# Kernel optimization log

Measured on AMD Instinct MI355X. Metric: run time of the kernel, lower is better.

Reference implementation:

```python
import jax, jax.numpy as jnp
import numpy as np

B, S, H, F, E, TOPK = 2, 1024, 1024, 2816, 8, 2

def setup_inputs() -> dict:
    key = jax.random.key(0)
    k1, k2, k3, k4 = jax.random.split(key, 4)
    return {
        "hidden_states": jax.random.normal(k1, (B, S, H), dtype=jnp.float32),
        "gate_w": jax.random.normal(k2, (E, H), dtype=jnp.float32) * 0.02,  # gate 1x1 conv == [E,H] matrix
        "w1": jax.random.normal(k3, (E, F, H), dtype=jnp.float32) * 0.02,   # per-expert up-proj
        "w2": jax.random.normal(k4, (E, H, F), dtype=jnp.float32) * 0.02,   # per-expert down-proj
        "top_k": TOPK,
    }

def reference(hidden_states, gate_w, w1, w2, top_k):
    b, s, h = hidden_states.shape
    e = gate_w.shape[0]
    x = hidden_states.reshape(-1, h)                       # [N, H]
    n = x.shape[0]
    # Router: 1x1 conv gate == linear, softmax, top-k, renormalize
    logits = x @ gate_w.T                                  # [N, E]
    probs = jax.nn.softmax(logits, axis=-1)
    topw, topi = jax.lax.top_k(probs, top_k)               # [N, k]
    topw = topw / jnp.sum(topw, axis=-1, keepdims=True)
    # Per-(token, expert) combine weight; zero for non-selected experts.
    # Equivalent to torch.where(topk_indices == e, topk_weights, 0).sum(-1).
    comb = jnp.zeros((n, e), dtype=x.dtype).at[jnp.arange(n)[:, None], topi].add(topw)  # [N, E]
    # Expert MLPs (1x1 convs == GEMMs): up -> SiLU -> down, weighted combine.
    up = jnp.einsum('nh,efh->nef', x, w1)                  # [N, E, F]
    act = jax.nn.silu(up)
    out = jnp.einsum('nef,ehf->neh', act, w2)              # [N, E, H]
    y = jnp.einsum('ne,neh->nh', comb, out)                # weighted combine
    return y.reshape(b, s, h)
```

## Files before the change

kernel.cpp:

```cpp
#include <hip/hip_runtime.h>
#include <stdint.h>

#define N_TOK 2048
#define H_DIM 1024
#define F_DIM 2816
#define N_EXP 8
#define NSLOT (N_TOK * 2)

#define BK 64
#define KSPLIT 2
#define KHALF (F_DIM / KSPLIT)
#define MAX_TILES 40

#define NU_W (N_EXP * F_DIM * H_DIM / 8)

typedef __attribute__((ext_vector_type(8))) short bf16x8;
typedef __attribute__((ext_vector_type(4))) float f32x4;

typedef __attribute__((address_space(1))) unsigned int gu32;
typedef __attribute__((address_space(3))) unsigned int lu32;

static __device__ __forceinline__ unsigned short f2bf(float f) {
    union { float f; unsigned u; } v; v.f = f;
    unsigned r = v.u + 0x7fffu + ((v.u >> 16) & 1u);
    return (unsigned short)(r >> 16);
}

static __device__ __forceinline__ void gload16(const unsigned short* g, unsigned short* l) {
    __builtin_amdgcn_global_load_lds((const gu32*)g, (lu32*)l, 16, 0, 0);
}

static __device__ __forceinline__ void conv8(const float* __restrict__ src,
                                             unsigned short* __restrict__ dst, long k)
{
    const float4 a = *(const float4*)(src + k * 8);
    const float4 b = *(const float4*)(src + k * 8 + 4);
    uint4 o;
    o.x = (unsigned)f2bf(a.x) | ((unsigned)f2bf(a.y) << 16);
    o.y = (unsigned)f2bf(a.z) | ((unsigned)f2bf(a.w) << 16);
    o.z = (unsigned)f2bf(b.x) | ((unsigned)f2bf(b.y) << 16);
    o.w = (unsigned)f2bf(b.z) | ((unsigned)f2bf(b.w) << 16);
    *(uint4*)(dst + k * 8) = o;
}

__global__ __launch_bounds__(256) void convert_w_kernel(
    const float* __restrict__ w1, const float* __restrict__ w2,
    unsigned short* __restrict__ w1_bf, unsigned short* __restrict__ w2_bf)
{
    const long total = 2L * NU_W;
    long u = ((long)blockIdx.x * 256 + threadIdx.x) * 2;
    const long stride = (long)gridDim.x * 256 * 2;
    for (; u < total; u += stride) {
        const float* src = (u < NU_W) ? w1 : w2;
        unsigned short* dst = (u < NU_W) ? w1_bf : w2_bf;
        const long k = (u < NU_W) ? u : u - NU_W;
        conv8(src, dst, k);
        conv8(src, dst, k + 1);
    }
}

__global__ __launch_bounds__(256) void router_kernel(
    const float* __restrict__ x, const float* __restrict__ gate_w,
    int* __restrict__ counts, int* __restrict__ row_token, float* __restrict__ row_weight,
    int* __restrict__ slot_e, int* __restrict__ slot_pos,
    unsigned short* __restrict__ x_bf)
{
    __shared__ float gsm[N_EXP * H_DIM];
    for (int i = threadIdx.x; i < N_EXP * H_DIM / 4; i += 256)
        ((float4*)gsm)[i] = ((const float4*)gate_w)[i];
    __syncthreads();

    const int wave = threadIdx.x >> 6;
    const int lane = threadIdx.x & 63;
    const int n = blockIdx.x * 4 + wave;
    if (n >= N_TOK) return;

    const float4* xrow = (const float4*)(x + (size_t)n * H_DIM);
    float4 xv[4];
#pragma unroll
    for (int i = 0; i < 4; i++) xv[i] = xrow[lane + 64 * i];

#pragma unroll
    for (int i = 0; i < 4; i++) {
        ushort4 b;
        b.x = f2bf(xv[i].x); b.y = f2bf(xv[i].y); b.z = f2bf(xv[i].z); b.w = f2bf(xv[i].w);
        *(ushort4*)(x_bf + (size_t)n * H_DIM + (lane + 64 * i) * 4) = b;
    }

    float logit[N_EXP];
#pragma unroll
    for (int e = 0; e < N_EXP; e++) {
        float p = 0.f;
#pragma unroll
        for (int i = 0; i < 4; i++) {
            const float4 g = ((const float4*)gsm)[e * 256 + lane + 64 * i];
            p += xv[i].x * g.x + xv[i].y * g.y + xv[i].z * g.z + xv[i].w * g.w;
        }
#pragma unroll
        for (int s = 32; s > 0; s >>= 1) p += __shfl_xor(p, s, 64);
        logit[e] = p;
    }

    if (lane == 0) {
        int e0 = 0; float l0 = logit[0];
#pragma unroll
        for (int e = 1; e < N_EXP; e++) if (logit[e] > l0) { l0 = logit[e]; e0 = e; }
        int e1 = -1; float l1 = -3.4e38f;
#pragma unroll
        for (int e = 0; e < N_EXP; e++) if (e != e0 && logit[e] > l1) { l1 = logit[e]; e1 = e; }
        float w0 = 1.f / (1.f + __expf(l1 - l0));
        float w1 = 1.f - w0;
        int p0 = atomicAdd(&counts[e0], 1);
        int p1 = atomicAdd(&counts[e1], 1);
        row_token[e0 * N_TOK + p0] = n;  row_weight[e0 * N_TOK + p0] = w0;
        row_token[e1 * N_TOK + p1] = n;  row_weight[e1 * N_TOK + p1] = w1;
        slot_e[n * 2 + 0] = e0;  slot_pos[n * 2 + 0] = p0;
        slot_e[n * 2 + 1] = e1;  slot_pos[n * 2 + 1] = p1;
    }
}

__global__ void scan_kernel(const int* __restrict__ counts, int* __restrict__ offsets,
                            int* __restrict__ tile_e, int* __restrict__ tile_m,
                            int* __restrict__ ntiles)
{
    if (threadIdx.x == 0 && blockIdx.x == 0) {
        int acc = 0, t = 0;
        for (int e = 0; e < N_EXP; e++) {
            offsets[e] = acc; acc += counts[e];
            const int nt = (counts[e] + 127) >> 7;
            for (int m = 0; m < nt; m++) { tile_e[t] = e; tile_m[t] = m; t++; }
        }
        *ntiles = t;
    }
}

__global__ __launch_bounds__(256) void up_gemm_kernel(
    const unsigned short* __restrict__ x_bf, const unsigned short* __restrict__ w1_bf,
    const int* __restrict__ counts, const int* __restrict__ offsets,
    const int* __restrict__ tile_e, const int* __restrict__ tile_m,
    const int* __restrict__ ntiles,
    const int* __restrict__ row_token,
    unsigned short* __restrict__ act)
{
    const int slot = blockIdx.y;
    if (slot >= *ntiles) return;
    const int e = tile_e[slot];
    const int mTile = tile_m[slot];
    const int cnt = counts[e];
    const int fTile = blockIdx.x;
    const int off = offsets[e];

    __shared__ __align__(16) unsigned short As[128 * 64];
    __shared__ __align__(16) unsigned short Bs[128 * 64];

    const int tid = threadIdx.x;
    const int lane = tid & 63;
    const int wave = tid >> 6;
    const int wm = (wave >> 1) * 64, wn = (wave & 1) * 64;

    const unsigned short* aSrc[4];
    const unsigned short* bSrc[4];
#pragma unroll
    for (int j = 0; j < 4; j++) {
        const int row_local = wave * 32 + j * 8 + (lane >> 3);
        const int pos = mTile * 128 + row_local;
        const int tok = row_token[e * N_TOK + min(pos, cnt - 1)];
        aSrc[j] = x_bf + (size_t)tok * H_DIM + (lane & 7) * 8;
        bSrc[j] = w1_bf + ((size_t)e * F_DIM + fTile * 128 + row_local) * H_DIM + (lane & 7) * 8;
    }

    f32x4 acc[4][4];
#pragma unroll
    for (int i = 0; i < 4; i++)
#pragma unroll
        for (int j = 0; j < 4; j++) acc[i][j] = (f32x4)(0.f);

    const int NKT = H_DIM / BK;
    for (int kt = 0; kt < NKT; kt++) {
        const int koff = kt * BK;
#pragma unroll
        for (int j = 0; j < 4; j++) {
            gload16(aSrc[j] + koff, As + (wave * 4 + j) * 512);
            gload16(bSrc[j] + koff, Bs + (wave * 4 + j) * 512);
        }
        __syncthreads();
#pragma unroll
        for (int kk = 0; kk < BK / 32; kk++) {
            const int kloc = kk * 32 + (lane >> 4) * 8;
            bf16x8 af[4], bfr[4];
#pragma unroll
            for (int i = 0; i < 4; i++)
                af[i] = *(const bf16x8*)(As + (wm + i * 16 + (lane & 15)) * 64 + kloc);
#pragma unroll
            for (int i = 0; i < 4; i++)
                bfr[i] = *(const bf16x8*)(Bs + (wn + i * 16 + (lane & 15)) * 64 + kloc);
#pragma unroll
            for (int i = 0; i < 4; i++)
#pragma unroll
                for (int j = 0; j < 4; j++)
                    acc[i][j] = __builtin_amdgcn_mfma_f32_16x16x32_bf16(af[i], bfr[j], acc[i][j], 0, 0, 0);
        }
        __syncthreads();
    }

#pragma unroll
    for (int i = 0; i < 4; i++) {
        const int mrow = wm + i * 16 + ((lane >> 4) << 2);
#pragma unroll
        for (int r = 0; r < 4; r++) {
            const int m = mTile * 128 + mrow + r;
            if (m < cnt) {
#pragma unroll
                for (int j = 0; j < 4; j++) {
                    float v = acc[i][j][r];
                    float s = v / (1.f + __expf(-v));
                    int col = fTile * 128 + wn + j * 16 + (lane & 15);
                    act[(size_t)(off + m) * F_DIM + col] = f2bf(s);
                }
            }
        }
    }
}

__global__ __launch_bounds__(256) void down_gemm_kernel(
    const unsigned short* __restrict__ act, const unsigned short* __restrict__ w2_bf,
    const int* __restrict__ counts, const int* __restrict__ offsets,
    const int* __restrict__ tile_e, const int* __restrict__ tile_m,
    const int* __restrict__ ntiles,
    const float* __restrict__ row_weight,
    float* __restrict__ out_partial)
{
    const int slot = blockIdx.y;
    if (slot >= *ntiles) return;
    const int e = tile_e[slot];
    const int mTile = tile_m[slot];
    const int ks = blockIdx.z;
    const int cnt = counts[e];
    const int hTile = blockIdx.x;
    const int off = offsets[e];
    const int kbase = ks * KHALF;

    __shared__ __align__(16) unsigned short As[128 * 64];
    __shared__ __align__(16) unsigned short Bs[128 * 64];

    const int tid = threadIdx.x;
    const int lane = tid & 63;
    const int wave = tid >> 6;
    const int wm = (wave >> 1) * 64, wn = (wave & 1) * 64;

    const unsigned short* aSrc[4];
    const unsigned short* bSrc[4];
#pragma unroll
    for (int j = 0; j < 4; j++) {
        const int row_local = wave * 32 + j * 8 + (lane >> 3);
        const int slotRow = off + min(mTile * 128 + row_local, cnt - 1);
        aSrc[j] = act + (size_t)slotRow * F_DIM + kbase + (lane & 7) * 8;
        bSrc[j] = w2_bf + ((size_t)e * H_DIM + hTile * 128 + row_local) * F_DIM + kbase + (lane & 7) * 8;
    }

    f32x4 acc[4][4];
#pragma unroll
    for (int i = 0; i < 4; i++)
#pragma unroll
        for (int j = 0; j < 4; j++) acc[i][j] = (f32x4)(0.f);

    const int NKT = KHALF / BK;
    for (int kt = 0; kt < NKT; kt++) {
        const int koff = kt * BK;
#pragma unroll
        for (int j = 0; j < 4; j++) {
            gload16(aSrc[j] + koff, As + (wave * 4 + j) * 512);
            gload16(bSrc[j] + koff, Bs + (wave * 4 + j) * 512);
        }
        __syncthreads();
#pragma unroll
        for (int kk = 0; kk < BK / 32; kk++) {
            const int kloc = kk * 32 + (lane >> 4) * 8;
            bf16x8 af[4], bfr[4];
#pragma unroll
            for (int i = 0; i < 4; i++)
                af[i] = *(const bf16x8*)(As + (wm + i * 16 + (lane & 15)) * 64 + kloc);
#pragma unroll
            for (int i = 0; i < 4; i++)
                bfr[i] = *(const bf16x8*)(Bs + (wn + i * 16 + (lane & 15)) * 64 + kloc);
#pragma unroll
            for (int i = 0; i < 4; i++)
#pragma unroll
                for (int j = 0; j < 4; j++)
                    acc[i][j] = __builtin_amdgcn_mfma_f32_16x16x32_bf16(af[i], bfr[j], acc[i][j], 0, 0, 0);
        }
        __syncthreads();
    }

    float* obase = out_partial + (size_t)ks * NSLOT * H_DIM;
#pragma unroll
    for (int i = 0; i < 4; i++) {
        const int mrow = wm + i * 16 + ((lane >> 4) << 2);
#pragma unroll
        for (int r = 0; r < 4; r++) {
            const int m = mTile * 128 + mrow + r;
            if (m < cnt) {
                const float w = row_weight[e * N_TOK + m];
#pragma unroll
                for (int j = 0; j < 4; j++) {
                    int col = hTile * 128 + wn + j * 16 + (lane & 15);
                    obase[(size_t)(off + m) * H_DIM + col] = w * acc[i][j][r];
                }
            }
        }
    }
}

__global__ __launch_bounds__(256) void combine_kernel(
    const float* __restrict__ out_partial, const int* __restrict__ offsets,
    const int* __restrict__ slot_e, const int* __restrict__ slot_pos,
    float* __restrict__ out)
{
    const int n = blockIdx.x;
    const int r0 = offsets[slot_e[n * 2 + 0]] + slot_pos[n * 2 + 0];
    const int r1 = offsets[slot_e[n * 2 + 1]] + slot_pos[n * 2 + 1];
    const int t = threadIdx.x;
    const float* p0 = out_partial;
    const float* p1 = out_partial + (size_t)NSLOT * H_DIM;
    const float4 a = *(const float4*)(p0 + (size_t)r0 * H_DIM + t * 4);
    const float4 b = *(const float4*)(p1 + (size_t)r0 * H_DIM + t * 4);
    const float4 c = *(const float4*)(p0 + (size_t)r1 * H_DIM + t * 4);
    const float4 d = *(const float4*)(p1 + (size_t)r1 * H_DIM + t * 4);
    float4 s;
    s.x = (a.x + b.x) + (c.x + d.x);
    s.y = (a.y + b.y) + (c.y + d.y);
    s.z = (a.z + b.z) + (c.z + d.z);
    s.w = (a.w + b.w) + (c.w + d.w);
    *(float4*)(out + (size_t)n * H_DIM + t * 4) = s;
}

extern "C" void kernel_launch(void* const* d_in, const int* in_sizes, int n_in,
                              void* d_out, int out_size, void* d_ws, size_t ws_size,
                              hipStream_t stream) {
    const float* x      = (const float*)d_in[0];
    const float* gate_w = (const float*)d_in[1];
    const float* w1     = (const float*)d_in[2];
    const float* w2     = (const float*)d_in[3];
    float* out = (float*)d_out;

    char* ws = (char*)d_ws;
    size_t o = 0;
    auto alloc = [&](size_t bytes) -> void* {
        void* p = ws + o;
        o = (o + bytes + 255) & ~(size_t)255;
        return p;
    };
    int*   counts     = (int*)  alloc(N_EXP * sizeof(int));
    int*   offsets    = (int*)  alloc(N_EXP * sizeof(int));
    int*   tile_e     = (int*)  alloc(MAX_TILES * sizeof(int));
    int*   tile_m     = (int*)  alloc(MAX_TILES * sizeof(int));
    int*   ntiles     = (int*)  alloc(sizeof(int));
    int*   row_token  = (int*)  alloc((size_t)N_EXP * N_TOK * sizeof(int));
    float* row_weight = (float*)alloc((size_t)N_EXP * N_TOK * sizeof(float));
    int*   slot_e     = (int*)  alloc((size_t)N_TOK * 2 * sizeof(int));
    int*   slot_pos   = (int*)  alloc((size_t)N_TOK * 2 * sizeof(int));
    unsigned short* act = (unsigned short*)alloc((size_t)NSLOT * F_DIM * sizeof(unsigned short));
    float* out_partial = (float*)alloc((size_t)KSPLIT * NSLOT * H_DIM * sizeof(float));
    unsigned short* x_bf  = (unsigned short*)alloc((size_t)N_TOK * H_DIM * sizeof(unsigned short));
    unsigned short* w1_bf = (unsigned short*)alloc((size_t)N_EXP * F_DIM * H_DIM * sizeof(unsigned short));
    unsigned short* w2_bf = (unsigned short*)alloc((size_t)N_EXP * H_DIM * F_DIM * sizeof(unsigned short));

    hipMemsetAsync(counts, 0, N_EXP * sizeof(int), stream);

    router_kernel<<<N_TOK / 4, 256, 0, stream>>>(x, gate_w, counts, row_token, row_weight, slot_e, slot_pos, x_bf);
    scan_kernel<<<1, 64, 0, stream>>>(counts, offsets, tile_e, tile_m, ntiles);
    convert_w_kernel<<<4096, 256, 0, stream>>>(w1, w2, w1_bf, w2_bf);
    up_gemm_kernel<<<dim3(F_DIM / 128, MAX_TILES), 256, 0, stream>>>(
        x_bf, w1_bf, counts, offsets, tile_e, tile_m, ntiles, row_token, act);
    down_gemm_kernel<<<dim3(H_DIM / 128, MAX_TILES, KSPLIT), 256, 0, stream>>>(
        act, w2_bf, counts, offsets, tile_e, tile_m, ntiles, row_weight, out_partial);
    combine_kernel<<<N_TOK, 256, 0, stream>>>(out_partial, offsets, slot_e, slot_pos, out);
}
```

Measured before the change: 397.9 us.

## Enlarge expert GEMM M-tile to 256 rows with 512-thread blocks

Both expert GEMMs now use 256x128 tiles computed by 8 waves (each 128x32), so each block reuses the loaded weight tile across twice as many token rows. This halves redundant weight streaming from global memory and reduces the tile count, with MAX_TILES dropping to 24. The weight conversion kernel now processes one float4 per thread iteration on a smaller grid. The risks are more padding waste on partial expert tiles, fewer blocks in flight, and higher per-wave A-fragment LDS reads.

```diff
diff --git a/kernel.cpp b/kernel.cpp
--- a/kernel.cpp
+++ b/kernel.cpp
@@ -10,9 +10,7 @@
 #define BK 64
 #define KSPLIT 2
 #define KHALF (F_DIM / KSPLIT)
-#define MAX_TILES 40
-
-#define NU_W (N_EXP * F_DIM * H_DIM / 8)
+#define MAX_TILES 24
 
 typedef __attribute__((ext_vector_type(8))) short bf16x8;
 typedef __attribute__((ext_vector_type(4))) float f32x4;
@@ -30,32 +28,21 @@
     __builtin_amdgcn_global_load_lds((const gu32*)g, (lu32*)l, 16, 0, 0);
 }
 
-static __device__ __forceinline__ void conv8(const float* __restrict__ src,
-                                             unsigned short* __restrict__ dst, long k)
-{
-    const float4 a = *(const float4*)(src + k * 8);
-    const float4 b = *(const float4*)(src + k * 8 + 4);
-    uint4 o;
-    o.x = (unsigned)f2bf(a.x) | ((unsigned)f2bf(a.y) << 16);
-    o.y = (unsigned)f2bf(a.z) | ((unsigned)f2bf(a.w) << 16);
-    o.z = (unsigned)f2bf(b.x) | ((unsigned)f2bf(b.y) << 16);
-    o.w = (unsigned)f2bf(b.z) | ((unsigned)f2bf(b.w) << 16);
-    *(uint4*)(dst + k * 8) = o;
-}
-
 __global__ __launch_bounds__(256) void convert_w_kernel(
     const float* __restrict__ w1, const float* __restrict__ w2,
     unsigned short* __restrict__ w1_bf, unsigned short* __restrict__ w2_bf)
 {
-    const long total = 2L * NU_W;
-    long u = ((long)blockIdx.x * 256 + threadIdx.x) * 2;
-    const long stride = (long)gridDim.x * 256 * 2;
-    for (; u < total; u += stride) {
-        const float* src = (u < NU_W) ? w1 : w2;
-        unsigned short* dst = (u < NU_W) ? w1_bf : w2_bf;
-        const long k = (u < NU_W) ? u : u - NU_W;
-        conv8(src, dst, k);
-        conv8(src, dst, k + 1);
+    const long NU4 = (long)N_EXP * F_DIM * H_DIM / 4;
+    const long total = 2 * NU4;
+    for (long u = (long)blockIdx.x * 256 + threadIdx.x; u < total; u += (long)gridDim.x * 256) {
+        const float* src = (u < NU4) ? w1 : w2;
+        unsigned short* dst = (u < NU4) ? w1_bf : w2_bf;
+        const long k = (u < NU4) ? u : u - NU4;
+        const float4 v = *(const float4*)(src + k * 4);
+        uint2 o;
+        o.x = (unsigned)f2bf(v.x) | ((unsigned)f2bf(v.y) << 16);
+        o.y = (unsigned)f2bf(v.z) | ((unsigned)f2bf(v.w) << 16);
+        *(uint2*)(dst + k * 4) = o;
     }
 }
 
@@ -127,14 +114,14 @@
         int acc = 0, t = 0;
         for (int e = 0; e < N_EXP; e++) {
             offsets[e] = acc; acc += counts[e];
-            const int nt = (counts[e] + 127) >> 7;
+            const int nt = (counts[e] + 255) >> 8;
             for (int m = 0; m < nt; m++) { tile_e[t] = e; tile_m[t] = m; t++; }
         }
         *ntiles = t;
     }
 }
 
-__global__ __launch_bounds__(256) void up_gemm_kernel(
+__global__ __launch_bounds__(512, 2) void up_gemm_kernel(
     const unsigned short* __restrict__ x_bf, const unsigned short* __restrict__ w1_bf,
     const int* __restrict__ counts, const int* __restrict__ offsets,
     const int* __restrict__ tile_e, const int* __restrict__ tile_m,
@@ -150,68 +137,74 @@
     const int fTile = blockIdx.x;
     const int off = offsets[e];
 
-    __shared__ __align__(16) unsigned short As[128 * 64];
+    __shared__ __align__(16) unsigned short As[256 * 64];
     __shared__ __align__(16) unsigned short Bs[128 * 64];
 
     const int tid = threadIdx.x;
     const int lane = tid & 63;
     const int wave = tid >> 6;
-    const int wm = (wave >> 1) * 64, wn = (wave & 1) * 64;
+    const int wm = (wave >> 2) * 128;
+    const int wn = (wave & 3) * 32;
 
     const unsigned short* aSrc[4];
-    const unsigned short* bSrc[4];
+    const unsigned short* bSrc[2];
 #pragma unroll
     for (int j = 0; j < 4; j++) {
         const int row_local = wave * 32 + j * 8 + (lane >> 3);
-        const int pos = mTile * 128 + row_local;
+        const int pos = mTile * 256 + row_local;
         const int tok = row_token[e * N_TOK + min(pos, cnt - 1)];
         aSrc[j] = x_bf + (size_t)tok * H_DIM + (lane & 7) * 8;
+    }
+#pragma unroll
+    for (int j = 0; j < 2; j++) {
+        const int row_local = wave * 16 + j * 8 + (lane >> 3);
         bSrc[j] = w1_bf + ((size_t)e * F_DIM + fTile * 128 + row_local) * H_DIM + (lane & 7) * 8;
     }
 
-    f32x4 acc[4][4];
-#pragma unroll
-    for (int i = 0; i < 4; i++)
-#pragma unroll
-        for (int j = 0; j < 4; j++) acc[i][j] = (f32x4)(0.f);
+    f32x4 acc[8][2];
+#pragma unroll
+    for (int i = 0; i < 8; i++)
+#pragma unroll
+        for (int j = 0; j < 2; j++) acc[i][j] = (f32x4)(0.f);
 
     const int NKT = H_DIM / BK;
     for (int kt = 0; kt < NKT; kt++) {
         const int koff = kt * BK;
 #pragma unroll
-        for (int j = 0; j < 4; j++) {
+        for (int j = 0; j < 4; j++)
             gload16(aSrc[j] + koff, As + (wave * 4 + j) * 512);
-            gload16(bSrc[j] + koff, Bs + (wave * 4 + j) * 512);
-        }
+#pragma unroll
+        for (int j = 0; j < 2; j++)
+            gload16(bSrc[j] + koff, Bs + (wave * 2 + j) * 512);
         __syncthreads();
 #pragma unroll
         for (int kk = 0; kk < BK / 32; kk++) {
             const int kloc = kk * 32 + (lane >> 4) * 8;
-            bf16x8 af[4], bfr[4];
-#pragma unroll
-            for (int i = 0; i < 4; i++)
+            bf16x8 af[8], bfr[2];
+#pragma unroll
+            for (int i = 0; i < 8; i++)
                 af[i] = *(const bf16x8*)(As + (wm + i * 16 + (lane & 15)) * 64 + kloc);
 #pragma unroll
-            for (int i = 0; i < 4; i++)
-                bfr[i] = *(const bf16x8*)(Bs + (wn + i * 16 + (lane & 15)) * 64 + kloc);
-#pragma unroll
-            for (int i = 0; i < 4; i++)
-#pragma unroll
-                for (int j = 0; j < 4; j++)
+            for (int j = 0; j < 2; j++)
+                bfr[j] = *(const bf16x8*)(Bs + (wn + j * 16 + (lane & 15)) * 64 + kloc);
+#pragma unroll
+            for (int i = 0; i < 8; i++)
+#pragma unroll
+                for (int j = 0; j < 2; j++)
                     acc[i][j] = __builtin_amdgcn_mfma_f32_16x16x32_bf16(af[i], bfr[j], acc[i][j], 0, 0, 0);
         }
         __syncthreads();
     }
 
 #pragma unroll
-    for (int i = 0; i < 4; i++) {
+    for (int i = 0; i < 8; i++) {
         const int mrow = wm + i * 16 + ((lane >> 4) << 2);
 #pragma unroll
         for (int r = 0; r < 4; r++) {
-            const int m = mTile * 128 + mrow + r;
+            const int m = mTile * 256 + mrow + r;
             if (m < cnt) {
 #pragma unroll
-                for (int j = 0; j < 4; j++) {
+                for (int j = 0; j < 2; j++) {
                     float v = acc[i][j][r];
                     float s = v / (1.f + __expf(-v));
                     int col = fTile * 128 + wn + j * 16 + (lane & 15);
@@ -222,7 +215,7 @@
     }
 }
 
-__global__ __launch_bounds__(256) void down_gemm_kernel(
+__global__ __launch_bounds__(512, 2) void down_gemm_kernel(
     const unsigned short* __restrict__ act, const unsigned short* __restrict__ w2_bf,
     const int* __restrict__ counts, const int* __restrict__ offsets,
     const int* __restrict__ tile_e, const int* __restrict__ tile_m,
@@ -240,53 +233,59 @@
     const int off = offsets[e];
     const int kbase = ks * KHALF;
 
-    __shared__ __align__(16) unsigned short As[128 * 64];
+    __shared__ __align__(16) unsigned short As[256 * 64];
     __shared__ __align__(16) unsigned short Bs[128 * 64];
 
     const int tid = threadIdx.x;
     const int lane = tid & 63;
     const int wave = tid >> 6;
-    const int wm = (wave >> 1) * 64, wn = (wave & 1) * 64;
+    const int wm = (wave >> 2) * 128;
+    const int wn = (wave & 3) * 32;
 
     const unsigned short* aSrc[4];
-    const unsigned short* bSrc[4];
+    const unsigned short* bSrc[2];
 #pragma unroll
     for (int j = 0; j < 4; j++) {
         const int row_local = wave * 32 + j * 8 + (lane >> 3);
-        const int slotRow = off + min(mTile * 128 + row_local, cnt - 1);
+        const int slotRow = off + min(mTile * 256 + row_local, cnt - 1);
         aSrc[j] = act + (size_t)slotRow * F_DIM + kbase + (lane & 7) * 8;
+    }
+#pragma unroll
+    for (int j = 0; j < 2; j++) {
+        const int row_local = wave * 16 + j * 8 + (lane >> 3);
         bSrc[j] = w2_bf + ((size_t)e * H_DIM + hTile * 128 + row_local) * F_DIM + kbase + (lane & 7) * 8;
     }
 
-    f32x4 acc[4][4];
-#pragma unroll
-    for (int i = 0; i < 4; i++)
-#pragma unroll
-        for (int j = 0; j < 4; j++) acc[i][j] = (f32x4)(0.f);
+    f32x4 acc[8][2];
+#pragma unroll
+    for (int i = 0; i < 8; i++)
+#pragma unroll
+        for (int j = 0; j < 2; j++) acc[i][j] = (f32x4)(0.f);
 
     const int NKT = KHALF / BK;
     for (int kt = 0; kt < NKT; kt++) {
         const int koff = kt * BK;
 #pragma unroll
-        for (int j = 0; j < 4; j++) {
+        for (int j = 0; j < 4; j++)
             gload16(aSrc[j] + koff, As + (wave * 4 + j) * 512);
-            gload16(bSrc[j] + koff, Bs + (wave * 4 + j) * 512);
-        }
+#pragma unroll
+        for (int j = 0; j < 2; j++)
+            gload16(bSrc[j] + koff, Bs + (wave * 2 + j) * 512);
         __syncthreads();
 #pragma unroll
         for (int kk = 0; kk < BK / 32; kk++) {
             const int kloc = kk * 32 + (lane >> 4) * 8;
-            bf16x8 af[4], bfr[4];
-#pragma unroll
-            for (int i = 0; i < 4; i++)
+            bf16x8 af[8], bfr[2];
+#pragma unroll
+            for (int i = 0; i < 8; i++)
                 af[i] = *(const bf16x8*)(As + (wm + i * 16 + (lane & 15)) * 64 + kloc);
 #pragma unroll
-            for (int i = 0; i < 4; i++)
-                bfr[i] = *(const bf16x8*)(Bs + (wn + i * 16 + (lane & 15)) * 64 + kloc);
-#pragma unroll
-            for (int i = 0; i < 4; i++)
-#pragma unroll
-                for (int j = 0; j < 4; j++)
+            for (int j = 0; j < 2; j++)
+                bfr[j] = *(const bf16x8*)(Bs + (wn + j * 16 + (lane & 15)) * 64 + kloc);
+#pragma unroll
+            for (int i = 0; i < 8; i++)
+#pragma unroll
+                for (int j = 0; j < 2; j++)
                     acc[i][j] = __builtin_amdgcn_mfma_f32_16x16x32_bf16(af[i], bfr[j], acc[i][j], 0, 0, 0);
         }
         __syncthreads();
@@ -294,15 +293,15 @@
 
     float* obase = out_partial + (size_t)ks * NSLOT * H_DIM;
 #pragma unroll
-    for (int i = 0; i < 4; i++) {
+    for (int i = 0; i < 8; i++) {
         const int mrow = wm + i * 16 + ((lane >> 4) << 2);
 #pragma unroll
         for (int r = 0; r < 4; r++) {
-            const int m = mTile * 128 + mrow + r;
+            const int m = mTile * 256 + mrow + r;
             if (m < cnt) {
                 const float w = row_weight[e * N_TOK + m];
 #pragma unroll
-                for (int j = 0; j < 4; j++) {
+                for (int j = 0; j < 2; j++) {
                     int col = hTile * 128 + wn + j * 16 + (lane & 15);
                     obase[(size_t)(off + m) * H_DIM + col] = w * acc[i][j][r];
                 }
@@ -369,10 +368,10 @@
 
     router_kernel<<<N_TOK / 4, 256, 0, stream>>>(x, gate_w, counts, row_token, row_weight, slot_e, slot_pos, x_bf);
     scan_kernel<<<1, 64, 0, stream>>>(counts, offsets, tile_e, tile_m, ntiles);
-    convert_w_kernel<<<4096, 256, 0, stream>>>(w1, w2, w1_bf, w2_bf);
-    up_gemm_kernel<<<dim3(F_DIM / 128, MAX_TILES), 256, 0, stream>>>(
+    convert_w_kernel<<<2048, 256, 0, stream>>>(w1, w2, w1_bf, w2_bf);
+    up_gemm_kernel<<<dim3(F_DIM / 128, MAX_TILES), 512, 0, stream>>>(
         x_bf, w1_bf, counts, offsets, tile_e, tile_m, ntiles, row_token, act);
-    down_gemm_kernel<<<dim3(H_DIM / 128, MAX_TILES, KSPLIT), 256, 0, stream>>>(
+    down_gemm_kernel<<<dim3(H_DIM / 128, MAX_TILES, KSPLIT), 512, 0, stream>>>(
         act, w2_bf, counts, offsets, tile_e, tile_m, ntiles, row_weight, out_partial);
     combine_kernel<<<N_TOK, 256, 0, stream>>>(out_partial, offsets, slot_e, slot_pos, out);
 }
```

Measured after the change: 414.3 us. 1.04x slower.

## Double-buffer LDS in expert GEMMs and fold scan into weight conversion

Applied to the files above, without the earlier changes.

Both up and down expert GEMMs now prefetch the next K tile into a second LDS buffer while computing on the current one, with raised wave priority around the MFMA section. The separate single-thread scan kernel is merged into the weight-conversion kernel, removing one launch, and the conversion loop is reworked to process float4 chunks with a halved grid. This aims to hide global-to-LDS latency behind matrix math, at the cost of doubling LDS per block, which may lower occupancy.

```diff
diff --git a/kernel.cpp b/kernel.cpp
--- a/kernel.cpp
+++ b/kernel.cpp
@@ -12,8 +12,6 @@
 #define KHALF (F_DIM / KSPLIT)
 #define MAX_TILES 40
 
-#define NU_W (N_EXP * F_DIM * H_DIM / 8)
-
 typedef __attribute__((ext_vector_type(8))) short bf16x8;
 typedef __attribute__((ext_vector_type(4))) float f32x4;
 
@@ -30,32 +28,53 @@
     __builtin_amdgcn_global_load_lds((const gu32*)g, (lu32*)l, 16, 0, 0);
 }
 
-static __device__ __forceinline__ void conv8(const float* __restrict__ src,
-                                             unsigned short* __restrict__ dst, long k)
-{
-    const float4 a = *(const float4*)(src + k * 8);
-    const float4 b = *(const float4*)(src + k * 8 + 4);
-    uint4 o;
-    o.x = (unsigned)f2bf(a.x) | ((unsigned)f2bf(a.y) << 16);
-    o.y = (unsigned)f2bf(a.z) | ((unsigned)f2bf(a.w) << 16);
-    o.z = (unsigned)f2bf(b.x) | ((unsigned)f2bf(b.y) << 16);
-    o.w = (unsigned)f2bf(b.z) | ((unsigned)f2bf(b.w) << 16);
-    *(uint4*)(dst + k * 8) = o;
-}
-
 __global__ __launch_bounds__(256) void convert_w_kernel(
     const float* __restrict__ w1, const float* __restrict__ w2,
-    unsigned short* __restrict__ w1_bf, unsigned short* __restrict__ w2_bf)
+    unsigned short* __restrict__ w1_bf, unsigned short* __restrict__ w2_bf,
+    const int* __restrict__ counts, int* __restrict__ offsets,
+    int* __restrict__ tile_e, int* __restrict__ tile_m, int* __restrict__ ntiles)
 {
-    const long total = 2L * NU_W;
-    long u = ((long)blockIdx.x * 256 + threadIdx.x) * 2;
-    const long stride = (long)gridDim.x * 256 * 2;
-    for (; u < total; u += stride) {
-        const float* src = (u < NU_W) ? w1 : w2;
-        unsigned short* dst = (u < NU_W) ? w1_bf : w2_bf;
-        const long k = (u < NU_W) ? u : u - NU_W;
-        conv8(src, dst, k);
-        conv8(src, dst, k + 1);
+    if (blockIdx.x == 0 && threadIdx.x == 0) {
+        int acc = 0, t = 0;
+        for (int e = 0; e < N_EXP; e++) {
+            offsets[e] = acc; acc += counts[e];
+            const int nt = (counts[e] + 127) >> 7;
+            for (int m = 0; m < nt; m++) { tile_e[t] = e; tile_m[t] = m; t++; }
+        }
+        *ntiles = t;
+    }
+
+    const long NU4 = (long)N_EXP * F_DIM * H_DIM / 4;
+    const long total = 2 * NU4;
+    long u = (long)blockIdx.x * 256 + threadIdx.x;
+    const long stride = (long)gridDim.x * 256;
+    for (; u + stride < total; u += 2 * stride) {
+        const long u1 = u + stride;
+        const float* s0 = (u  < NU4) ? w1 : w2;
+        const float* s1 = (u1 < NU4) ? w1 : w2;
+        unsigned short* d0 = (u  < NU4) ? w1_bf : w2_bf;
+        unsigned short* d1 = (u1 < NU4) ? w1_bf : w2_bf;
+        const long k0 = (u  < NU4) ? u  : u  - NU4;
+        const long k1 = (u1 < NU4) ? u1 : u1 - NU4;
+        const float4 v0 = *(const float4*)(s0 + k0 * 4);
+        const float4 v1 = *(const float4*)(s1 + k1 * 4);
+        uint2 o0, o1;
+        o0.x = (unsigned)f2bf(v0.x) | ((unsigned)f2bf(v0.y) << 16);
+        o0.y = (unsigned)f2bf(v0.z) | ((unsigned)f2bf(v0.w) << 16);
+        o1.x = (unsigned)f2bf(v1.x) | ((unsigned)f2bf(v1.y) << 16);
+        o1.y = (unsigned)f2bf(v1.z) | ((unsigned)f2bf(v1.w) << 16);
+        *(uint2*)(d0 + k0 * 4) = o0;
+        *(uint2*)(d1 + k1 * 4) = o1;
+    }
+    if (u < total) {
+        const float* s = (u < NU4) ? w1 : w2;
+        unsigned short* d = (u < NU4) ? w1_bf : w2_bf;
+        const long k = (u < NU4) ? u : u - NU4;
+        const float4 v = *(const float4*)(s + k * 4);
+        uint2 o;
+        o.x = (unsigned)f2bf(v.x) | ((unsigned)f2bf(v.y) << 16);
+        o.y = (unsigned)f2bf(v.z) | ((unsigned)f2bf(v.w) << 16);
+        *(uint2*)(d + k * 4) = o;
     }
 }
 
@@ -116,21 +135,6 @@
         row_token[e1 * N_TOK + p1] = n;  row_weight[e1 * N_TOK + p1] = w1;
         slot_e[n * 2 + 0] = e0;  slot_pos[n * 2 + 0] = p0;
         slot_e[n * 2 + 1] = e1;  slot_pos[n * 2 + 1] = p1;
-    }
-}
-
-__global__ void scan_kernel(const int* __restrict__ counts, int* __restrict__ offsets,
-                            int* __restrict__ tile_e, int* __restrict__ tile_m,
-                            int* __restrict__ ntiles)
-{
-    if (threadIdx.x == 0 && blockIdx.x == 0) {
-        int acc = 0, t = 0;
-        for (int e = 0; e < N_EXP; e++) {
-            offsets[e] = acc; acc += counts[e];
-            const int nt = (counts[e] + 127) >> 7;
-            for (int m = 0; m < nt; m++) { tile_e[t] = e; tile_m[t] = m; t++; }
-        }
-        *ntiles = t;
     }
 }
 
@@ -150,8 +154,8 @@
     const int fTile = blockIdx.x;
     const int off = offsets[e];
 
-    __shared__ __align__(16) unsigned short As[128 * 64];
-    __shared__ __align__(16) unsigned short Bs[128 * 64];
+    __shared__ __align__(16) unsigned short As[2][128 * 64];
+    __shared__ __align__(16) unsigned short Bs[2][128 * 64];
 
     const int tid = threadIdx.x;
     const int lane = tid & 63;
@@ -175,31 +179,42 @@
 #pragma unroll
         for (int j = 0; j < 4; j++) acc[i][j] = (f32x4)(0.f);
 
+#pragma unroll
+    for (int j = 0; j < 4; j++) {
+        gload16(aSrc[j], &As[0][(wave * 4 + j) * 512]);
+        gload16(bSrc[j], &Bs[0][(wave * 4 + j) * 512]);
+    }
+    __syncthreads();
+
     const int NKT = H_DIM / BK;
     for (int kt = 0; kt < NKT; kt++) {
-        const int koff = kt * BK;
-#pragma unroll
-        for (int j = 0; j < 4; j++) {
-            gload16(aSrc[j] + koff, As + (wave * 4 + j) * 512);
-            gload16(bSrc[j] + koff, Bs + (wave * 4 + j) * 512);
-        }
-        __syncthreads();
+        const int cur = kt & 1;
+        if (kt + 1 < NKT) {
+            const int koff = (kt + 1) * BK;
+#pragma unroll
+            for (int j = 0; j < 4; j++) {
+                gload16(aSrc[j] + koff, &As[cur ^ 1][(wave * 4 + j) * 512]);
+                gload16(bSrc[j] + koff, &Bs[cur ^ 1][(wave * 4 + j) * 512]);
+            }
+        }
+        __builtin_amdgcn_s_setprio(1);
 #pragma unroll
         for (int kk = 0; kk < BK / 32; kk++) {
             const int kloc = kk * 32 + (lane >> 4) * 8;
             bf16x8 af[4], bfr[4];
 #pragma unroll
             for (int i = 0; i < 4; i++)
-                af[i] = *(const bf16x8*)(As + (wm + i * 16 + (lane & 15)) * 64 + kloc);
-#pragma unroll
-            for (int i = 0; i < 4; i++)
-                bfr[i] = *(const bf16x8*)(Bs + (wn + i * 16 + (lane & 15)) * 64 + kloc);
+                af[i] = *(const bf16x8*)(&As[cur][(wm + i * 16 + (lane & 15)) * 64 + kloc]);
+#pragma unroll
+            for (int i = 0; i < 4; i++)
+                bfr[i] = *(const bf16x8*)(&Bs[cur][(wn + i * 16 + (lane & 15)) * 64 + kloc]);
 #pragma unroll
             for (int i = 0; i < 4; i++)
 #pragma unroll
                 for (int j = 0; j < 4; j++)
                     acc[i][j] = __builtin_amdgcn_mfma_f32_16x16x32_bf16(af[i], bfr[j], acc[i][j], 0, 0, 0);
         }
+        __builtin_amdgcn_s_setprio(0);
         __syncthreads();
     }
 
@@ -240,8 +255,8 @@
     const int off = offsets[e];
     const int kbase = ks * KHALF;
 
-    __shared__ __align__(16) unsigned short As[128 * 64];
-    __shared__ __align__(16) unsigned short Bs[128 * 64];
+    __shared__ __align__(16) unsigned short As[2][128 * 64];
+    __shared__ __align__(16) unsigned short Bs[2][128 * 64];
 
     const int tid = threadIdx.x;
     const int lane = tid & 63;
@@ -264,31 +279,42 @@
 #pragma unroll
         for (int j = 0; j < 4; j++) acc[i][j] = (f32x4)(0.f);
 
+#pragma unroll
+    for (int j = 0; j < 4; j++) {
+        gload16(aSrc[j], &As[0][(wave * 4 + j) * 512]);
+        gload16(bSrc[j], &Bs[0][(wave * 4 + j) * 512]);
+    }
+    __syncthreads();
+
     const int NKT = KHALF / BK;
     for (int kt = 0; kt < NKT; kt++) {
-        const int koff = kt * BK;
-#pragma unroll
-        for (int j = 0; j < 4; j++) {
-            gload16(aSrc[j] + koff, As + (wave * 4 + j) * 512);
-            gload16(bSrc[j] + koff, Bs + (wave * 4 + j) * 512);
-        }
-        __syncthreads();
+        const int cur = kt & 1;
+        if (kt + 1 < NKT) {
+            const int koff = (kt + 1) * BK;
+#pragma unroll
+            for (int j = 0; j < 4; j++) {
+                gload16(aSrc[j] + koff, &As[cur ^ 1][(wave * 4 + j) * 512]);
+                gload16(bSrc[j] + koff, &Bs[cur ^ 1][(wave * 4 + j) * 512]);
+            }
+        }
+        __builtin_amdgcn_s_setprio(1);
 #pragma unroll
         for (int kk = 0; kk < BK / 32; kk++) {
             const int kloc = kk * 32 + (lane >> 4) * 8;
             bf16x8 af[4], bfr[4];
 #pragma unroll
             for (int i = 0; i < 4; i++)
-                af[i] = *(const bf16x8*)(As + (wm + i * 16 + (lane & 15)) * 64 + kloc);
-#pragma unroll
-            for (int i = 0; i < 4; i++)
-                bfr[i] = *(const bf16x8*)(Bs + (wn + i * 16 + (lane & 15)) * 64 + kloc);
+                af[i] = *(const bf16x8*)(&As[cur][(wm + i * 16 + (lane & 15)) * 64 + kloc]);
+#pragma unroll
+            for (int i = 0; i < 4; i++)
+                bfr[i] = *(const bf16x8*)(&Bs[cur][(wn + i * 16 + (lane & 15)) * 64 + kloc]);
 #pragma unroll
             for (int i = 0; i < 4; i++)
 #pragma unroll
                 for (int j = 0; j < 4; j++)
                     acc[i][j] = __builtin_amdgcn_mfma_f32_16x16x32_bf16(af[i], bfr[j], acc[i][j], 0, 0, 0);
         }
+        __builtin_amdgcn_s_setprio(0);
         __syncthreads();
     }
 
@@ -368,8 +394,8 @@
     hipMemsetAsync(counts, 0, N_EXP * sizeof(int), stream);
 
     router_kernel<<<N_TOK / 4, 256, 0, stream>>>(x, gate_w, counts, row_token, row_weight, slot_e, slot_pos, x_bf);
-    scan_kernel<<<1, 64, 0, stream>>>(counts, offsets, tile_e, tile_m, ntiles);
-    convert_w_kernel<<<4096, 256, 0, stream>>>(w1, w2, w1_bf, w2_bf);
+    convert_w_kernel<<<2048, 256, 0, stream>>>(w1, w2, w1_bf, w2_bf,
+                                               counts, offsets, tile_e, tile_m, ntiles);
     up_gemm_kernel<<<dim3(F_DIM / 128, MAX_TILES), 256, 0, stream>>>(
         x_bf, w1_bf, counts, offsets, tile_e, tile_m, ntiles, row_token, act);
     down_gemm_kernel<<<dim3(H_DIM / 128, MAX_TILES, KSPLIT), 256, 0, stream>>>(
```

Result: slower. 417.6 us (+5.0%).
